# Kernel optimization log

Measured on AMD Instinct MI355X. Metric: run time of the kernel, lower is better.

The kernel has to match this reference:

```python
import jax, jax.numpy as jnp
import numpy as np
import math

B, S, IN_DIM, FEATURES = 4, 4096, 1024, 1024


def setup_inputs() -> dict:
    key = jax.random.key(0)
    kx, kk = jax.random.split(key)
    x = jax.random.normal(kx, (B, S, IN_DIM), dtype=jnp.float32)
    # bool kernel representing a +1/-1 binary weight matrix
    kernel = jax.random.randint(kk, (IN_DIM, FEATURES), 0, 2).astype(jnp.bool_)
    scale = jnp.float32(1.0 / math.sqrt(IN_DIM))  # nn.initializers.constant(1/sqrt(in_dim))
    return {"x": x, "kernel": kernel, "scale": scale}


def reference(x, kernel, scale):
    # conn_dense: bool kernel encodes +1 (True) / -1 (False) weights
    w = jnp.where(kernel, 1.0, -1.0).astype(x.dtype)  # [in_dim, features]
    # [b, s, in] @ [in, f] -> [b, s, f], then scalar scale
    return scale * jnp.einsum("bsi,if->bsf", x, w)
```

## Files before the change

### kernel.cpp

```cpp
#include <hip/hip_runtime.h>


#define M_TOT 16384
#define N_TOT 1024
#define K_TOT 1024

typedef __attribute__((ext_vector_type(8))) short bf16x8;
typedef __attribute__((ext_vector_type(4))) float f32x4;

__device__ __forceinline__ unsigned short f2bf(float f) {
    unsigned int u = __builtin_bit_cast(unsigned int, f);
    u += 0x7FFFu + ((u >> 16) & 1u);
    return (unsigned short)(u >> 16);
}

__global__ __launch_bounds__(256) void prep(
    const void* __restrict__ w_raw, unsigned short* __restrict__ wt,
    const float4* __restrict__ x, ushort4* __restrict__ xb)
{
    __shared__ unsigned short tile[64 * 72];
    __shared__ int smode;
    const int tid = threadIdx.x;

    if (blockIdx.x >= 256) {
        const int S = 4096 * 256;
        int g = (blockIdx.x - 256) * 256 + tid;
        #pragma unroll
        for (int j = 0; j < 4; ++j) {
            int idx = g + j * S;
            float4 v = x[idx];
            ushort4 h;
            h.x = f2bf(v.x); h.y = f2bf(v.y); h.z = f2bf(v.z); h.w = f2bf(v.w);
            xb[idx] = h;
        }
        return;
    }

    const int k0 = (blockIdx.x & 15) * 64;
    const int n0 = (blockIdx.x >> 4) * 64;
    const int row = tid >> 2;
    const int seg = (tid & 3) * 16;

    if (tid == 0) smode = 0;
    __syncthreads();
    {
        const unsigned int* k32 = (const unsigned int*)w_raw;
        int bad = 0;
        for (int i = tid; i < 1024; i += 256)
            bad |= (k32[i] > 1u) ? 1 : 0;
        if (bad) atomicOr(&smode, 1);
    }
    __syncthreads();

    if (smode == 0) {
        const unsigned int* w = (const unsigned int*)w_raw;
        const uint4* src = reinterpret_cast<const uint4*>(
            w + (size_t)(k0 + row) * N_TOT + n0 + seg);
        #pragma unroll
        for (int q = 0; q < 4; ++q) {
            uint4 v = src[q];
            ushort4 h;
            h.x = v.x ? 0x3F80u : 0xBF80u;
            h.y = v.y ? 0x3F80u : 0xBF80u;
            h.z = v.z ? 0x3F80u : 0xBF80u;
            h.w = v.w ? 0x3F80u : 0xBF80u;
            *reinterpret_cast<ushort4*>(&tile[row * 72 + seg + q * 4]) = h;
        }
    } else {
        const unsigned char* w = (const unsigned char*)w_raw;
        uint4 v = *reinterpret_cast<const uint4*>(
            w + (size_t)(k0 + row) * N_TOT + n0 + seg);
        unsigned char b[16];
        *reinterpret_cast<uint4*>(b) = v;
        #pragma unroll
        for (int q = 0; q < 4; ++q) {
            ushort4 h;
            h.x = b[q * 4 + 0] ? 0x3F80u : 0xBF80u;
            h.y = b[q * 4 + 1] ? 0x3F80u : 0xBF80u;
            h.z = b[q * 4 + 2] ? 0x3F80u : 0xBF80u;
            h.w = b[q * 4 + 3] ? 0x3F80u : 0xBF80u;
            *reinterpret_cast<ushort4*>(&tile[row * 72 + seg + q * 4]) = h;
        }
    }
    __syncthreads();
    {
        int n = tid >> 2, kseg = (tid & 3) * 16;
        ushort4 o[4];
        #pragma unroll
        for (int j = 0; j < 16; ++j)
            ((unsigned short*)o)[j] = tile[(kseg + j) * 72 + n];
        ushort4* dst = reinterpret_cast<ushort4*>(wt + (size_t)(n0 + n) * K_TOT + k0 + kseg);
        dst[0] = o[0]; dst[1] = o[1]; dst[2] = o[2]; dst[3] = o[3];
    }
}

__global__ __launch_bounds__(256) void bf16_gemm(
    const unsigned short* __restrict__ A,
    const unsigned short* __restrict__ BT,
    const float* __restrict__ scale_p, float* __restrict__ out)
{
    __shared__ unsigned short As[128 * 64];
    __shared__ unsigned short Bs[128 * 64];

    const int tid  = threadIdx.x;
    const int lane = tid & 63;
    const int wave = tid >> 6;
    const int wm = (wave & 1) * 64;
    const int wn = (wave >> 1) * 64;

    const int j  = blockIdx.x & 7;
    const int s  = blockIdx.x >> 3;
    const int by = ((s >> 3) << 3) | j;
    const int bx = s & 7;
    const int m0 = by * 128, n0 = bx * 128;

    const int fr = lane & 15, fq = lane >> 4;
    const float scale = scale_p[0];

    const int srow = wave * 32 + (lane >> 3);
    const int skch = (lane & 7) ^ (lane >> 3);

    f32x4 acc[4][4] = {};

    for (int k0 = 0; k0 < K_TOT; k0 += 64) {
        #pragma unroll
        for (int q = 0; q < 4; ++q) {
            const unsigned short* g = A + (size_t)(m0 + srow + q * 8) * K_TOT + k0 + skch * 8;
            __builtin_amdgcn_global_load_lds(
                (const __attribute__((address_space(1))) void*)g,
                (__attribute__((address_space(3))) void*)&As[wave * 2048 + q * 512],
                16, 0, 0);
        }
        #pragma unroll
        for (int q = 0; q < 4; ++q) {
            const unsigned short* g = BT + (size_t)(n0 + srow + q * 8) * K_TOT + k0 + skch * 8;
            __builtin_amdgcn_global_load_lds(
                (const __attribute__((address_space(1))) void*)g,
                (__attribute__((address_space(3))) void*)&Bs[wave * 2048 + q * 512],
                16, 0, 0);
        }
        __syncthreads();

        #pragma unroll
        for (int ks = 0; ks < 2; ++ks) {
            bf16x8 af[4], bfr[4];
            #pragma unroll
            for (int mi = 0; mi < 4; ++mi) {
                int r  = wm + mi * 16 + fr;
                int ch = (ks * 4 + fq) ^ (r & 7);
                af[mi] = *reinterpret_cast<const bf16x8*>(&As[r * 64 + ch * 8]);
            }
            #pragma unroll
            for (int ni = 0; ni < 4; ++ni) {
                int r  = wn + ni * 16 + fr;
                int ch = (ks * 4 + fq) ^ (r & 7);
                bfr[ni] = *reinterpret_cast<const bf16x8*>(&Bs[r * 64 + ch * 8]);
            }
            #pragma unroll
            for (int mi = 0; mi < 4; ++mi)
                #pragma unroll
                for (int ni = 0; ni < 4; ++ni)
                    acc[mi][ni] = __builtin_amdgcn_mfma_f32_16x16x32_bf16(
                        af[mi], bfr[ni], acc[mi][ni], 0, 0, 0);
        }
        __syncthreads();
    }

    #pragma unroll
    for (int mi = 0; mi < 4; ++mi) {
        #pragma unroll
        for (int ni = 0; ni < 4; ++ni) {
            const int col  = n0 + wn + ni * 16 + fr;
            const int rowb = m0 + wm + mi * 16 + fq * 4;
            #pragma unroll
            for (int jj = 0; jj < 4; ++jj)
                out[(size_t)(rowb + jj) * N_TOT + col] = scale * acc[mi][ni][jj];
        }
    }
}

#define BKP 40
__global__ __launch_bounds__(256, 2) void binary_dense_gemm(
    const float* __restrict__ x, const int* __restrict__ kern,
    const float* __restrict__ scale_p, float* __restrict__ out)
{
    __shared__ unsigned short Asf[128 * BKP];
    __shared__ unsigned short Bsf[128 * BKP];
    const int tid = threadIdx.x, lane = tid & 63, wave = tid >> 6;
    const int wm = (wave & 1) * 64, wn = (wave >> 1) * 64;
    const int bx = blockIdx.x & 7, by = blockIdx.x >> 3;
    const int m0 = by * 128, n0 = bx * 128;
    const float scale = scale_p[0];
    const int fr = lane & 15, fq = lane >> 4;
    f32x4 acc[4][4] = {};
    for (int k0 = 0; k0 < K_TOT; k0 += 32) {
        #pragma unroll
        for (int i = 0; i < 4; ++i) {
            int slot = tid + i * 256, row = slot >> 3, kg = (slot & 7) << 2;
            const float4 v = *reinterpret_cast<const float4*>(x + (size_t)(m0 + row) * K_TOT + k0 + kg);
            ushort4 h;
            h.x = f2bf(v.x); h.y = f2bf(v.y); h.z = f2bf(v.z); h.w = f2bf(v.w);
            *reinterpret_cast<ushort4*>(&Asf[row * BKP + kg]) = h;
        }
        #pragma unroll
        for (int i = 0; i < 4; ++i) {
            int slot = tid + i * 256, nl = slot & 127, kg = (slot >> 7) << 2;
            ushort4 h;
            h.x = kern[(size_t)(k0 + kg + 0) * N_TOT + n0 + nl] ? 0x3F80u : 0xBF80u;
            h.y = kern[(size_t)(k0 + kg + 1) * N_TOT + n0 + nl] ? 0x3F80u : 0xBF80u;
            h.z = kern[(size_t)(k0 + kg + 2) * N_TOT + n0 + nl] ? 0x3F80u : 0xBF80u;
            h.w = kern[(size_t)(k0 + kg + 3) * N_TOT + n0 + nl] ? 0x3F80u : 0xBF80u;
            *reinterpret_cast<ushort4*>(&Bsf[nl * BKP + kg]) = h;
        }
        __syncthreads();
        bf16x8 af[4], bfr[4];
        #pragma unroll
        for (int mi = 0; mi < 4; ++mi)
            af[mi] = *reinterpret_cast<const bf16x8*>(&Asf[(wm + mi * 16 + fr) * BKP + fq * 8]);
        #pragma unroll
        for (int ni = 0; ni < 4; ++ni)
            bfr[ni] = *reinterpret_cast<const bf16x8*>(&Bsf[(wn + ni * 16 + fr) * BKP + fq * 8]);
        #pragma unroll
        for (int mi = 0; mi < 4; ++mi)
            #pragma unroll
            for (int ni = 0; ni < 4; ++ni)
                acc[mi][ni] = __builtin_amdgcn_mfma_f32_16x16x32_bf16(af[mi], bfr[ni], acc[mi][ni], 0, 0, 0);
        __syncthreads();
    }
    #pragma unroll
    for (int mi = 0; mi < 4; ++mi)
        #pragma unroll
        for (int ni = 0; ni < 4; ++ni) {
            const int col = n0 + wn + ni * 16 + fr;
            const int rowb = m0 + wm + mi * 16 + fq * 4;
            #pragma unroll
            for (int jj = 0; jj < 4; ++jj)
                out[(size_t)(rowb + jj) * N_TOT + col] = scale * acc[mi][ni][jj];
        }
}

extern "C" void kernel_launch(void* const* d_in, const int* in_sizes, int n_in,
                              void* d_out, int out_size, void* d_ws, size_t ws_size,
                              hipStream_t stream) {
    const float* x     = (const float*)d_in[0];
    const void*  kern  = d_in[1];
    const float* scale = (const float*)d_in[2];
    float*       out   = (float*)d_out;

    const size_t xb_bytes = (size_t)M_TOT * K_TOT * 2;
    const size_t wt_bytes = (size_t)N_TOT * K_TOT * 2;
    const size_t xb_off   = 256;
    if (ws_size >= xb_off + xb_bytes + wt_bytes) {
        unsigned short* xb = (unsigned short*)((char*)d_ws + xb_off);
        unsigned short* wt = (unsigned short*)((char*)d_ws + xb_off + xb_bytes);
        hipLaunchKernelGGL(prep, dim3(256 + 4096), dim3(256), 0, stream,
                           kern, wt, (const float4*)x, (ushort4*)xb);
        hipLaunchKernelGGL(bf16_gemm, dim3(1024), dim3(256), 0, stream,
                           xb, wt, scale, out);
    } else {
        hipLaunchKernelGGL(binary_dense_gemm, dim3(1024), dim3(256), 0, stream,
                           x, (const int*)kern, scale, out);
    }
}
```

Before: 154.7 us.

## Fuse fp32-to-bf16 activation conversion into GEMM LDS load path

Removes the separate pass that converted x to bf16 in workspace. The GEMM now loads fp32 x tiles directly into swizzled LDS and converts to bf16 with packed convert instructions before MFMA. This eliminates the extra write and read of a bf16 copy of x, but doubles the global and LDS bytes for the A operand per tile, raises LDS usage, and adds conversion work in the inner loop.

After: 176.3 us. +14.0%, slower.

```diff
diff --git a/kernel.cpp b/kernel.cpp
--- a/kernel.cpp
+++ b/kernel.cpp
@@ -7,6 +7,7 @@
 
 typedef __attribute__((ext_vector_type(8))) short bf16x8;
 typedef __attribute__((ext_vector_type(4))) float f32x4;
+typedef __attribute__((ext_vector_type(4))) unsigned int u32x4;
 
 __device__ __forceinline__ unsigned short f2bf(float f) {
     unsigned int u = __builtin_bit_cast(unsigned int, f);
@@ -14,28 +15,18 @@
     return (unsigned short)(u >> 16);
 }
 
-__global__ __launch_bounds__(256) void prep(
-    const void* __restrict__ w_raw, unsigned short* __restrict__ wt,
-    const float4* __restrict__ x, ushort4* __restrict__ xb)
+__device__ __forceinline__ unsigned int cvt_pk_bf16(float a, float b) {
+    unsigned int r;
+    asm("v_cvt_pk_bf16_f32 %0, %1, %2" : "=v"(r) : "v"(a), "v"(b));
+    return r;
+}
+
+__global__ __launch_bounds__(256) void convert_w(
+    const void* __restrict__ w_raw, unsigned short* __restrict__ wt)
 {
     __shared__ unsigned short tile[64 * 72];
     __shared__ int smode;
     const int tid = threadIdx.x;
-
-    if (blockIdx.x >= 256) {
-        const int S = 4096 * 256;
-        int g = (blockIdx.x - 256) * 256 + tid;
-        #pragma unroll
-        for (int j = 0; j < 4; ++j) {
-            int idx = g + j * S;
-            float4 v = x[idx];
-            ushort4 h;
-            h.x = f2bf(v.x); h.y = f2bf(v.y); h.z = f2bf(v.z); h.w = f2bf(v.w);
-            xb[idx] = h;
-        }
-        return;
-    }
-
     const int k0 = (blockIdx.x & 15) * 64;
     const int n0 = (blockIdx.x >> 4) * 64;
     const int row = tid >> 2;
@@ -94,12 +85,12 @@
     }
 }
 
-__global__ __launch_bounds__(256) void bf16_gemm(
-    const unsigned short* __restrict__ A,
+__global__ __launch_bounds__(256) void fused_gemm(
+    const float* __restrict__ X,
     const unsigned short* __restrict__ BT,
     const float* __restrict__ scale_p, float* __restrict__ out)
 {
-    __shared__ unsigned short As[128 * 64];
+    __shared__ float          As[128 * 64];
     __shared__ unsigned short Bs[128 * 64];
 
     const int tid  = threadIdx.x;
@@ -120,15 +111,20 @@
     const int srow = wave * 32 + (lane >> 3);
     const int skch = (lane & 7) ^ (lane >> 3);
 
+    const int arow_l = lane >> 4;
+    const int adch   = lane & 15;
+
     f32x4 acc[4][4] = {};
 
     for (int k0 = 0; k0 < K_TOT; k0 += 64) {
         #pragma unroll
-        for (int q = 0; q < 4; ++q) {
-            const unsigned short* g = A + (size_t)(m0 + srow + q * 8) * K_TOT + k0 + skch * 8;
+        for (int q = 0; q < 8; ++q) {
+            const int r  = wave * 32 + q * 4 + arow_l;
+            const int sw = ((r & 7) << 1) | ((r >> 3) & 1);
+            const float* g = X + (size_t)(m0 + r) * K_TOT + k0 + ((adch ^ sw) << 2);
             __builtin_amdgcn_global_load_lds(
                 (const __attribute__((address_space(1))) void*)g,
-                (__attribute__((address_space(3))) void*)&As[wave * 2048 + q * 512],
+                (__attribute__((address_space(3))) void*)&As[(wave * 32 + q * 4) * 64],
                 16, 0, 0);
         }
         #pragma unroll
@@ -143,18 +139,27 @@
 
         #pragma unroll
         for (int ks = 0; ks < 2; ++ks) {
-            bf16x8 af[4], bfr[4];
-            #pragma unroll
-            for (int mi = 0; mi < 4; ++mi) {
-                int r  = wm + mi * 16 + fr;
-                int ch = (ks * 4 + fq) ^ (r & 7);
-                af[mi] = *reinterpret_cast<const bf16x8*>(&As[r * 64 + ch * 8]);
-            }
+            bf16x8 bfr[4];
             #pragma unroll
             for (int ni = 0; ni < 4; ++ni) {
                 int r  = wn + ni * 16 + fr;
                 int ch = (ks * 4 + fq) ^ (r & 7);
                 bfr[ni] = *reinterpret_cast<const bf16x8*>(&Bs[r * 64 + ch * 8]);
+            }
+            bf16x8 af[4];
+            #pragma unroll
+            for (int mi = 0; mi < 4; ++mi) {
+                int r  = wm + mi * 16 + fr;
+                int sw = ((r & 7) << 1) | ((r >> 3) & 1);
+                int g8 = ks * 4 + fq;
+                f32x4 lo = *reinterpret_cast<const f32x4*>(&As[r * 64 + (((2 * g8)     ^ sw) << 2)]);
+                f32x4 hi = *reinterpret_cast<const f32x4*>(&As[r * 64 + (((2 * g8 + 1) ^ sw) << 2)]);
+                u32x4 p;
+                p.x = cvt_pk_bf16(lo[0], lo[1]);
+                p.y = cvt_pk_bf16(lo[2], lo[3]);
+                p.z = cvt_pk_bf16(hi[0], hi[1]);
+                p.w = cvt_pk_bf16(hi[2], hi[3]);
+                af[mi] = __builtin_bit_cast(bf16x8, p);
             }
             #pragma unroll
             for (int mi = 0; mi < 4; ++mi)
@@ -247,16 +252,13 @@
     const float* scale = (const float*)d_in[2];
     float*       out   = (float*)d_out;
 
-    const size_t xb_bytes = (size_t)M_TOT * K_TOT * 2;
     const size_t wt_bytes = (size_t)N_TOT * K_TOT * 2;
-    const size_t xb_off   = 256;
-    if (ws_size >= xb_off + xb_bytes + wt_bytes) {
-        unsigned short* xb = (unsigned short*)((char*)d_ws + xb_off);
-        unsigned short* wt = (unsigned short*)((char*)d_ws + xb_off + xb_bytes);
-        hipLaunchKernelGGL(prep, dim3(256 + 4096), dim3(256), 0, stream,
-                           kern, wt, (const float4*)x, (ushort4*)xb);
-        hipLaunchKernelGGL(bf16_gemm, dim3(1024), dim3(256), 0, stream,
-                           xb, wt, scale, out);
+    const size_t wt_off   = 256;
+    if (ws_size >= wt_off + wt_bytes) {
+        unsigned short* wt = (unsigned short*)((char*)d_ws + wt_off);
+        hipLaunchKernelGGL(convert_w, dim3(256), dim3(256), 0, stream, kern, wt);
+        hipLaunchKernelGGL(fused_gemm, dim3(1024), dim3(256), 0, stream,
+                           x, wt, scale, out);
     } else {
         hipLaunchKernelGGL(binary_dense_gemm, dim3(1024), dim3(256), 0, stream,
                            x, (const int*)kern, scale, out);
```

## Replace bf16 GEMM with 256x256-tile, 8-wave, double-buffered pipelined kernel

Applied to the files above, without the earlier changes.

Replaces the 128x128-tile, 4-wave GEMM with a 256x256-tile, 512-thread kernel. It double-buffers LDS in 32-wide K halves and interleaves async global-to-LDS loads for the next tiles with MFMA phases, using fine-grained barriers, vmcnt waits and setprio. The aim is to hide global load latency behind compute and raise reuse per LDS byte. In exchange it uses more registers (128 accumulators per lane) and launches only 256 blocks, which may underfill the GPU and depends on the hand-tuned wait counts being correct.

Measured after the change: 155.7 us. No clear change (+0.7%).

```diff
diff --git a/kernel.cpp b/kernel.cpp
--- a/kernel.cpp
+++ b/kernel.cpp
@@ -94,84 +94,125 @@
     }
 }
 
-__global__ __launch_bounds__(256) void bf16_gemm(
+#define STAGE(P0, P1, LDSA, BUF, H, T) do {                                        \
+    const int _ko = (T) * 64 + (H) * 32;                                           \
+    __builtin_amdgcn_global_load_lds(                                              \
+        (const __attribute__((address_space(1))) void*)((P0) + _ko),               \
+        (__attribute__((address_space(3))) void*)&(LDSA)[((BUF)*2+(H))*8192 + dst0],\
+        16, 0, 0);                                                                 \
+    __builtin_amdgcn_global_load_lds(                                              \
+        (const __attribute__((address_space(1))) void*)((P1) + _ko),               \
+        (__attribute__((address_space(3))) void*)&(LDSA)[((BUF)*2+(H))*8192 + dst1],\
+        16, 0, 0);                                                                 \
+} while (0)
+
+__global__ __launch_bounds__(512, 2) void gemm8(
     const unsigned short* __restrict__ A,
     const unsigned short* __restrict__ BT,
     const float* __restrict__ scale_p, float* __restrict__ out)
 {
-    __shared__ unsigned short As[128 * 64];
-    __shared__ unsigned short Bs[128 * 64];
+    __shared__ unsigned short As[2 * 2 * 256 * 32];
+    __shared__ unsigned short Bs[2 * 2 * 256 * 32];
 
     const int tid  = threadIdx.x;
     const int lane = tid & 63;
     const int wave = tid >> 6;
-    const int wm = (wave & 1) * 64;
-    const int wn = (wave >> 1) * 64;
-
-    const int j  = blockIdx.x & 7;
-    const int s  = blockIdx.x >> 3;
-    const int by = ((s >> 3) << 3) | j;
-    const int bx = s & 7;
-    const int m0 = by * 128, n0 = bx * 128;
+    const int wr   = wave >> 2;
+    const int wc   = wave & 3;
+
+    const int g    = blockIdx.x;
+    const int by   = ((g >> 3) >> 2) * 8 + (g & 7);
+    const int bx   = (g >> 3) & 3;
+    const int m0   = by * 256, n0 = bx * 256;
 
     const int fr = lane & 15, fq = lane >> 4;
-    const float scale = scale_p[0];
-
-    const int srow = wave * 32 + (lane >> 3);
-    const int skch = (lane & 7) ^ (lane >> 3);
-
-    f32x4 acc[4][4] = {};
-
-    for (int k0 = 0; k0 < K_TOT; k0 += 64) {
-        #pragma unroll
-        for (int q = 0; q < 4; ++q) {
-            const unsigned short* g = A + (size_t)(m0 + srow + q * 8) * K_TOT + k0 + skch * 8;
-            __builtin_amdgcn_global_load_lds(
-                (const __attribute__((address_space(1))) void*)g,
-                (__attribute__((address_space(3))) void*)&As[wave * 2048 + q * 512],
-                16, 0, 0);
-        }
-        #pragma unroll
-        for (int q = 0; q < 4; ++q) {
-            const unsigned short* g = BT + (size_t)(n0 + srow + q * 8) * K_TOT + k0 + skch * 8;
-            __builtin_amdgcn_global_load_lds(
-                (const __attribute__((address_space(1))) void*)g,
-                (__attribute__((address_space(3))) void*)&Bs[wave * 2048 + q * 512],
-                16, 0, 0);
-        }
-        __syncthreads();
-
-        #pragma unroll
-        for (int ks = 0; ks < 2; ++ks) {
-            bf16x8 af[4], bfr[4];
-            #pragma unroll
-            for (int mi = 0; mi < 4; ++mi) {
-                int r  = wm + mi * 16 + fr;
-                int ch = (ks * 4 + fq) ^ (r & 7);
-                af[mi] = *reinterpret_cast<const bf16x8*>(&As[r * 64 + ch * 8]);
-            }
-            #pragma unroll
-            for (int ni = 0; ni < 4; ++ni) {
-                int r  = wn + ni * 16 + fr;
-                int ch = (ks * 4 + fq) ^ (r & 7);
-                bfr[ni] = *reinterpret_cast<const bf16x8*>(&Bs[r * 64 + ch * 8]);
-            }
-            #pragma unroll
-            for (int mi = 0; mi < 4; ++mi)
+
+    const int sd  = lane >> 2;
+    const int sc  = (lane & 3) ^ ((lane >> 3) & 3);
+    const int rr0 = wave * 32 + sd;
+    const int rr1 = rr0 + 16;
+    const unsigned short* pA0 = A  + (size_t)(m0 + rr0) * K_TOT + sc * 8;
+    const unsigned short* pA1 = A  + (size_t)(m0 + rr1) * K_TOT + sc * 8;
+    const unsigned short* pB0 = BT + (size_t)(n0 + rr0) * K_TOT + sc * 8;
+    const unsigned short* pB1 = BT + (size_t)(n0 + rr1) * K_TOT + sc * 8;
+    const int dst0 = wave * 1024;
+    const int dst1 = dst0 + 512;
+
+    const int chq  = fq ^ ((fr >> 1) & 3);
+    const int aoff = (wr * 128 + fr) * 32 + chq * 8;
+    const int boff = (wc * 64  + fr) * 32 + chq * 8;
+
+    f32x4 acc[8][4] = {};
+    bf16x8 bfr[4];
+
+    STAGE(pA0, pA1, As, 0, 0, 0);
+    STAGE(pB0, pB1, Bs, 0, 0, 0);
+    STAGE(pA0, pA1, As, 0, 1, 0);
+    STAGE(pB0, pB1, Bs, 0, 1, 0);
+    asm volatile("s_waitcnt vmcnt(4)" ::: "memory");
+    __builtin_amdgcn_s_barrier();
+
+    for (int i = 0; i < 8; ++i) {
+        const int to  = 2 * i + 1;
+        const int te2 = 2 * i + 2;
+        #pragma unroll
+        for (int p = 0; p < 8; ++p) {
+            const int rb = p >> 2;
+            const int kk = (p >> 1) & 1;
+            const int mh = p & 1;
+
+            bf16x8 af[4];
+            if (mh == 0) {
                 #pragma unroll
                 for (int ni = 0; ni < 4; ++ni)
-                    acc[mi][ni] = __builtin_amdgcn_mfma_f32_16x16x32_bf16(
-                        af[mi], bfr[ni], acc[mi][ni], 0, 0, 0);
-        }
-        __syncthreads();
-    }
-
+                    bfr[ni] = *reinterpret_cast<const bf16x8*>(
+                        &Bs[(rb * 2 + kk) * 8192 + boff + ni * 512]);
+            }
+            #pragma unroll
+            for (int mi2 = 0; mi2 < 4; ++mi2)
+                af[mi2] = *reinterpret_cast<const bf16x8*>(
+                    &As[(rb * 2 + kk) * 8192 + aoff + (mh * 4 + mi2) * 512]);
+
+            {
+                const int item = p & 3;
+                const int ts   = (p < 4) ? to : te2;
+                const int sb   = (p < 4) ? 1 : 0;
+                if (ts < 16) {
+                    const int h = item >> 1;
+                    if ((item & 1) == 0) STAGE(pA0, pA1, As, sb, h, ts);
+                    else                 STAGE(pB0, pB1, Bs, sb, h, ts);
+                }
+            }
+            __builtin_amdgcn_sched_barrier(0);
+            __builtin_amdgcn_s_barrier();
+            asm volatile("s_waitcnt lgkmcnt(0)" ::: "memory");
+            __builtin_amdgcn_sched_barrier(0);
+
+            __builtin_amdgcn_s_setprio(1);
+            #pragma unroll
+            for (int mi2 = 0; mi2 < 4; ++mi2)
+                #pragma unroll
+                for (int ni = 0; ni < 4; ++ni)
+                    acc[mh * 4 + mi2][ni] = __builtin_amdgcn_mfma_f32_16x16x32_bf16(
+                        af[mi2], bfr[ni], acc[mh * 4 + mi2][ni], 0, 0, 0);
+            __builtin_amdgcn_s_setprio(0);
+            __builtin_amdgcn_sched_barrier(0);
+
+            if (p & 1) {
+                if (i == 7 && p == 5) asm volatile("s_waitcnt vmcnt(0)" ::: "memory");
+                else                  asm volatile("s_waitcnt vmcnt(4)" ::: "memory");
+            }
+            __builtin_amdgcn_s_barrier();
+        }
+    }
+
+    const float scale = scale_p[0];
     #pragma unroll
-    for (int mi = 0; mi < 4; ++mi) {
+    for (int mi = 0; mi < 8; ++mi) {
         #pragma unroll
         for (int ni = 0; ni < 4; ++ni) {
-            const int col  = n0 + wn + ni * 16 + fr;
-            const int rowb = m0 + wm + mi * 16 + fq * 4;
+            const int col  = n0 + wc * 64 + ni * 16 + fr;
+            const int rowb = m0 + wr * 128 + mi * 16 + fq * 4;
             #pragma unroll
             for (int jj = 0; jj < 4; ++jj)
                 out[(size_t)(rowb + jj) * N_TOT + col] = scale * acc[mi][ni][jj];
@@ -255,7 +296,7 @@
         unsigned short* wt = (unsigned short*)((char*)d_ws + xb_off + xb_bytes);
         hipLaunchKernelGGL(prep, dim3(256 + 4096), dim3(256), 0, stream,
                            kern, wt, (const float4*)x, (ushort4*)xb);
-        hipLaunchKernelGGL(bf16_gemm, dim3(1024), dim3(256), 0, stream,
+        hipLaunchKernelGGL(gemm8, dim3(256), dim3(512), 0, stream,
                            xb, wt, scale, out);
     } else {
         hipLaunchKernelGGL(binary_dense_gemm, dim3(1024), dim3(256), 0, stream,
```
